# Performance work log

Measured on AMD Instinct MI355X. Metric: run time of the kernel, lower is better.

The kernel has to match this reference:

```python
import jax, jax.numpy as jnp
import numpy as np

N = 100000   # num entities / tail rows
D_IN = 128
D_OUT = 128
R = 8        # num relations
E = 131072   # edges per relation
B = 32768    # head entities per relation


def setup_inputs() -> dict:
    key = jax.random.key(0)
    ks = jax.random.split(key, 8)
    x = jax.random.normal(ks[0], (N, D_IN), dtype=jnp.float32)
    tail_rep = jax.random.normal(ks[1], (N, D_IN), dtype=jnp.float32)
    # Linear(in, out, bias=False) weight: [out, in], xavier-ish scale
    W = jax.random.normal(ks[2], (D_OUT, D_IN), dtype=jnp.float32) * (1.414 / np.sqrt(D_IN))
    # match_matrix embedding -> per-relation [in, out] matrices
    rel_W = jax.random.normal(ks[3], (R, D_IN, D_OUT), dtype=jnp.float32) * (1.0 / np.sqrt(D_IN))
    edge_weights = jax.random.uniform(ks[4], (R, E), dtype=jnp.float32)
    edge_rows = jax.random.randint(ks[5], (R, E), 0, B, dtype=jnp.int32)
    edge_cols = jax.random.randint(ks[6], (R, E), 0, N, dtype=jnp.int32)
    # head_indice: unique global entity ids per relation (torch code assigns by index)
    rng = np.random.default_rng(0)
    head = np.stack([rng.choice(N, size=B, replace=False) for _ in range(R)]).astype(np.int32)
    head_indice = jnp.asarray(head)
    return {"x": x, "tail_rep": tail_rep, "W": W, "rel_W": rel_W,
            "edge_weights": edge_weights, "edge_rows": edge_rows,
            "edge_cols": edge_cols, "head_indice": head_indice}


def reference(x, tail_rep, W, rel_W, edge_weights, edge_rows, edge_cols, head_indice):
    # emb_all = original_map(input)
    emb_all = x @ W.T                                   # [N, D_OUT]
    # per-relation dense transform of all tails: tail_rep @ rel_W[r]
    transformed = jnp.einsum('ni,rio->rno', tail_rep, rel_W)   # [R, N, D_OUT]
    # sparse.mm(sp_edge_e, all_rep_h): gather tail rows per edge, weight, segment-sum by local head row
    gathered = jnp.take_along_axis(transformed, edge_cols[:, :, None], axis=1)  # [R, E, D_OUT]
    contrib = edge_weights[:, :, None] * gathered                                # [R, E, D_OUT]
    seg = lambda c, rows: jax.ops.segment_sum(c, rows, num_segments=B)
    new_rep = jax.vmap(seg)(contrib, edge_rows)                                  # [R, B, D_OUT]
    # emb_all[ent_indice] = rel_update + emb_all[ent_indice]  (per relation, sequentially) == scatter-add
    emb_all = emb_all.at[head_indice.reshape(-1)].add(new_rep.reshape(-1, D_OUT))
    # activate=True
    return jax.nn.relu(emb_all)
```

## Files before the change

kernel.cpp:

```cpp
#include <hip/hip_runtime.h>
#include <hip/hip_bf16.h>

#define D_DIM 128
#define N_ENT 100000
#define R_REL 8
#define E_EDGE 131072
#define B_HEAD 32768
#define NH_PAD 100352
#define MAXE (R_REL * E_EDGE)

typedef __attribute__((ext_vector_type(8))) short short8v;
typedef __attribute__((ext_vector_type(16))) float f32x16;
typedef unsigned int uint;
typedef unsigned short ushort;

union BF8 {
  short8v v;
  __hip_bfloat16 h[8];
};

__device__ inline ushort bfbits(float x) {
  union { __hip_bfloat16 h; ushort u; } c;
  c.h = __float2bfloat16(x);
  return c.u;
}
__device__ inline float bflo(uint p) { return __uint_as_float(p << 16); }
__device__ inline float bfhi(uint p) { return __uint_as_float(p & 0xffff0000u); }

__global__ __launch_bounds__(256) void setup(int* __restrict__ cnt_e,
                                             int* __restrict__ inv,
                                             const float* __restrict__ W,
                                             const float* __restrict__ relW,
                                             short8v* __restrict__ WhS,
                                             const float* __restrict__ tail,
                                             short8v* __restrict__ tailb) {
  int bid = blockIdx.x;
  int tid = threadIdx.x;
  if (bid < 3136) {
    int i = bid * 256 + tid;
    if (i < R_REL * B_HEAD) cnt_e[i] = 0;
    inv[i] = -1;
  } else if (bid < 3208) {
    int b = bid - 3136;
    int mat = b >> 3;
    int idx = (b & 7) * 256 + tid;
    int o = idx & 127, ks = idx >> 7;
    float v[8];
    if (mat == 0) {
      const float* src = W + o * D_DIM + ks * 8;
#pragma unroll
      for (int j = 0; j < 8; ++j) v[j] = src[j];
    } else {
      const float* src =
          relW + (size_t)(mat - 1) * D_DIM * D_DIM + (ks * 8) * D_DIM + o;
#pragma unroll
      for (int j = 0; j < 8; ++j) v[j] = src[j * D_DIM];
    }
    BF8 h;
#pragma unroll
    for (int j = 0; j < 8; ++j) h.h[j] = __float2bfloat16(v[j]);
    WhS[(size_t)mat * 2048 + idx] = h.v;
  } else {
    int i = (bid - 3208) * 256 + tid;
    const float4* s = (const float4*)tail + (size_t)i * 2;
    float4 a = s[0], b = s[1];
    BF8 h;
    h.h[0] = __float2bfloat16(a.x); h.h[1] = __float2bfloat16(a.y);
    h.h[2] = __float2bfloat16(a.z); h.h[3] = __float2bfloat16(a.w);
    h.h[4] = __float2bfloat16(b.x); h.h[5] = __float2bfloat16(b.y);
    h.h[6] = __float2bfloat16(b.z); h.h[7] = __float2bfloat16(b.w);
    tailb[i] = h.v;
  }
}

__global__ __launch_bounds__(256) void hist_inv(const int* __restrict__ erow,
                                                const int* __restrict__ head,
                                                int* __restrict__ cnt,
                                                int* __restrict__ inv) {
  int bid = blockIdx.x;
  if (bid < 4096) {
    int r = bid >> 9;
    int e = (bid & 511) * 256 + threadIdx.x;
    int row = erow[(size_t)r * E_EDGE + e];
    atomicAdd(cnt + r * B_HEAD + row, 1);
  } else {
    int i = (bid - 4096) * 256 + threadIdx.x;
    int r = i >> 15;
    inv[r * NH_PAD + head[i]] = i & (B_HEAD - 1);
  }
}

__global__ __launch_bounds__(256) void scan_blk(const int* __restrict__ cnt,
                                                int* __restrict__ cur,
                                                int* __restrict__ bsum) {
  int b = blockIdx.x, t = threadIdx.x;
  int4 v = ((const int4*)cnt)[b * 256 + t];
  int s = v.x + v.y + v.z + v.w;
  __shared__ int ps[256];
  ps[t] = s;
  __syncthreads();
  for (int off = 1; off < 256; off <<= 1) {
    int u = (t >= off) ? ps[t - off] : 0;
    __syncthreads();
    ps[t] += u;
    __syncthreads();
  }
  int base = ps[t] - s;
  int4 o;
  o.x = base; o.y = base + v.x; o.z = o.y + v.y; o.w = o.z + v.z;
  ((int4*)cur)[b * 256 + t] = o;
  if (t == 255) bsum[b] = ps[255];
}

__global__ __launch_bounds__(256) void scan_bsum(int* __restrict__ bsum) {
  int t = threadIdx.x;
  int s = bsum[t];
  __shared__ int ps[256];
  ps[t] = s;
  __syncthreads();
  for (int off = 1; off < 256; off <<= 1) {
    int u = (t >= off) ? ps[t - off] : 0;
    __syncthreads();
    ps[t] += u;
    __syncthreads();
  }
  bsum[t] = ps[t] - s;
}

__global__ __launch_bounds__(256) void scatter_edges(const int* __restrict__ erow,
                                                     const int* __restrict__ ecol,
                                                     const float* __restrict__ ew,
                                                     int* __restrict__ cur,
                                                     const int* __restrict__ bsum,
                                                     int2* __restrict__ sColW) {
  int r = blockIdx.y;
  int e = blockIdx.x * 256 + threadIdx.x;
  size_t idx = (size_t)r * E_EDGE + e;
  int row = erow[idx];
  int gi = r * B_HEAD + row;
  int pos = atomicAdd(cur + gi, 1) + bsum[gi >> 10];
  sColW[pos] = make_int2(ecol[idx], __float_as_int(ew[idx]));
}

__global__ __launch_bounds__(256) void csr_agg(const uint* __restrict__ tailb,
                                               const int* __restrict__ cur_e,
                                               const int* __restrict__ cnt_e,
                                               const int* __restrict__ bsum,
                                               const int2* __restrict__ sColW,
                                               uint* __restrict__ aggb, int r0) {
  int base = (blockIdx.x << 3) + ((threadIdx.x >> 6) << 1);
  int lane = threadIdx.x & 63;
  int li = lane & 7;
  int f0 = r0 * B_HEAD + base, f1 = f0 + 1;
  int cn0 = cnt_e[f0], cn1 = cnt_e[f1];
  int s0 = cur_e[f0] - cn0 + bsum[f0 >> 10];
  int s1 = cur_e[f1] - cn1 + bsum[f1 >> 10];
  float a0x = 0.f, a0y = 0.f, a1x = 0.f, a1y = 0.f;
  int rounds = ((cn0 > cn1 ? cn0 : cn1) + 7) >> 3;
  for (int rr = 0; rr < rounds; ++rr) {
    int k = rr << 3;
    int i0 = k + li; if (i0 > cn0 - 1) i0 = cn0 > 0 ? cn0 - 1 : 0;
    int i1 = k + li; if (i1 > cn1 - 1) i1 = cn1 > 0 ? cn1 - 1 : 0;
    int g0 = s0 + i0; if (g0 > MAXE - 1) g0 = MAXE - 1;
    int g1 = s1 + i1; if (g1 > MAXE - 1) g1 = MAXE - 1;
    int2 ea = sColW[g0];
    int2 eb = sColW[g1];
#pragma unroll
    for (int j = 0; j < 8; ++j) {
      if (k + j < cn0) {
        int col = __shfl(ea.x, j, 8);
        float w = __int_as_float(__shfl(ea.y, j, 8));
        uint t = tailb[(size_t)col * 64 + lane];
        a0x += w * bflo(t); a0y += w * bfhi(t);
      }
      if (k + j < cn1) {
        int col = __shfl(eb.x, j, 8);
        float w = __int_as_float(__shfl(eb.y, j, 8));
        uint t = tailb[(size_t)col * 64 + lane];
        a1x += w * bflo(t); a1y += w * bfhi(t);
      }
    }
  }
  aggb[(size_t)base * 64 + lane] = (uint)bfbits(a0x) | ((uint)bfbits(a0y) << 16);
  aggb[(size_t)(base + 1) * 64 + lane] = (uint)bfbits(a1x) | ((uint)bfbits(a1y) << 16);
}

__global__ __launch_bounds__(256) void gemm_all(const float* __restrict__ x,
                                                const ushort* __restrict__ aggb,
                                                const short8v* __restrict__ WhS,
                                                float* __restrict__ out,
                                                ushort* __restrict__ updb, int r0,
                                                int nxb) {
  __shared__ short8v wlds[16][128];
  int tid = threadIdx.x;
  int bid = blockIdx.x;
  bool xpart = (bid < nxb);
  int mat, rowbase, relloc = 0;
  if (xpart) {
    mat = 0;
    rowbase = bid * 128;
  } else {
    int b = bid - nxb;
    relloc = b >> 8;
    mat = 1 + r0 + relloc;
    rowbase = (b & 255) * 128;
  }
  const short8v* Bsrc = WhS + (size_t)mat * 2048;
#pragma unroll
  for (int it = 0; it < 8; ++it) {
    int e = it * 256 + tid;
    wlds[e >> 7][e & 127] = Bsrc[e];
  }
  int w = tid >> 6, lane = tid & 63, lrow = lane & 31, lsel = lane >> 5;
  int arow = rowbase + w * 32 + lrow;
  f32x16 acc[4] = {};
  __syncthreads();

  if (xpart) {
    int arowc = (arow < N_ENT) ? arow : (N_ENT - 1);
    const float4* Arow = (const float4*)(x + (size_t)arowc * D_DIM);
#pragma unroll
    for (int kk = 0; kk < 8; ++kk) {
      float4 a0 = Arow[kk * 4 + lsel * 2];
      float4 a1 = Arow[kk * 4 + lsel * 2 + 1];
      BF8 ah;
      ah.h[0] = __float2bfloat16(a0.x); ah.h[1] = __float2bfloat16(a0.y);
      ah.h[2] = __float2bfloat16(a0.z); ah.h[3] = __float2bfloat16(a0.w);
      ah.h[4] = __float2bfloat16(a1.x); ah.h[5] = __float2bfloat16(a1.y);
      ah.h[6] = __float2bfloat16(a1.z); ah.h[7] = __float2bfloat16(a1.w);
      int ks = kk * 2 + lsel;
#pragma unroll
      for (int n = 0; n < 4; ++n)
        acc[n] = __builtin_amdgcn_mfma_f32_32x32x16_bf16(ah.v, wlds[ks][n * 32 + lrow],
                                                         acc[n], 0, 0, 0);
    }
    int wrow0 = rowbase + w * 32;
#pragma unroll
    for (int reg = 0; reg < 16; ++reg) {
      int srow = wrow0 + (reg & 3) + 8 * (reg >> 2) + 4 * lsel;
      if (srow < N_ENT) {
        float* orow = out + (size_t)srow * D_DIM;
#pragma unroll
        for (int n = 0; n < 4; ++n) orow[n * 32 + lrow] = acc[n][reg];
      }
    }
  } else {
    const short8v* Arow =
        (const short8v*)(aggb + ((size_t)relloc * B_HEAD + arow) * D_DIM);
#pragma unroll
    for (int kk = 0; kk < 8; ++kk) {
      short8v a = Arow[kk * 2 + lsel];
      int ks = kk * 2 + lsel;
#pragma unroll
      for (int n = 0; n < 4; ++n)
        acc[n] = __builtin_amdgcn_mfma_f32_32x32x16_bf16(a, wlds[ks][n * 32 + lrow],
                                                         acc[n], 0, 0, 0);
    }
    int wrow0 = rowbase + w * 32;
    ushort* ubase = updb + (size_t)relloc * B_HEAD * D_DIM;
#pragma unroll
    for (int reg = 0; reg < 16; ++reg) {
      int srow = wrow0 + (reg & 3) + 8 * (reg >> 2) + 4 * lsel;
      ushort* urow = ubase + (size_t)srow * D_DIM;
#pragma unroll
      for (int n = 0; n < 4; ++n) urow[n * 32 + lrow] = bfbits(acc[n][reg]);
    }
  }
}

__global__ __launch_bounds__(256) void final_add(const int* __restrict__ inv,
                                                 const ushort* __restrict__ updb,
                                                 float* __restrict__ out, int r0,
                                                 int c, int doRelu) {
  int n = blockIdx.x * 8 + (threadIdx.x >> 5);
  int lane = threadIdx.x & 31;
  if (n >= N_ENT) return;
  float4* o4 = (float4*)out + (size_t)n * 32 + lane;
  float4 v = *o4;
  for (int k = 0; k < c; ++k) {
    int row = inv[(r0 + k) * NH_PAD + n];
    if (row >= 0) {
      uint2 u = ((const uint2*)updb)[((size_t)k * B_HEAD + row) * 32 + lane];
      v.x += bflo(u.x); v.y += bfhi(u.x);
      v.z += bflo(u.y); v.w += bfhi(u.y);
    }
  }
  if (doRelu) {
    v.x = fmaxf(v.x, 0.f); v.y = fmaxf(v.y, 0.f);
    v.z = fmaxf(v.z, 0.f); v.w = fmaxf(v.w, 0.f);
  }
  *o4 = v;
}

extern "C" void kernel_launch(void* const* d_in, const int* in_sizes, int n_in,
                              void* d_out, int out_size, void* d_ws, size_t ws_size,
                              hipStream_t stream) {
  const float* x = (const float*)d_in[0];
  const float* tail = (const float*)d_in[1];
  const float* W = (const float*)d_in[2];
  const float* relW = (const float*)d_in[3];
  const float* ew = (const float*)d_in[4];
  const int* erow = (const int*)d_in[5];
  const int* ecol = (const int*)d_in[6];
  const int* head = (const int*)d_in[7];
  float* out = (float*)d_out;

  char* p = (char*)d_ws;
  short8v* WhS = (short8v*)p;   p += (size_t)(R_REL + 1) * 2048 * 16;
  short8v* tailb = (short8v*)p; p += (size_t)N_ENT * D_DIM * 2;
  int* cnt_e = (int*)p;         p += (size_t)R_REL * B_HEAD * 4;
  int* cur_e = (int*)p;         p += (size_t)R_REL * B_HEAD * 4;
  int* inv = (int*)p;           p += (size_t)R_REL * NH_PAD * 4;
  int* bsum = (int*)p;          p += 256 * 4;
  int2* sColW = (int2*)p;       p += (size_t)R_REL * E_EDGE * 8;
  char* dyn = p;
  size_t fixed = (size_t)(p - (char*)d_ws);
  size_t per_rel = (size_t)B_HEAD * D_DIM * 2 * 2;
  size_t avail = (ws_size > fixed) ? ws_size - fixed : 0;
  int chunk = (int)(avail / per_rel);
  if (chunk > R_REL) chunk = R_REL;
  if (chunk < 1) chunk = 1;
  ushort* aggb = (ushort*)dyn;
  ushort* updb = (ushort*)(dyn + (size_t)chunk * B_HEAD * D_DIM * 2);

  const int NXB = (N_ENT + 127) / 128;

  setup<<<dim3(3136 + 72 + 6250), 256, 0, stream>>>(cnt_e, inv, W, relW, WhS, tail,
                                                    tailb);
  hist_inv<<<dim3(4096 + R_REL * B_HEAD / 256), 256, 0, stream>>>(erow, head, cnt_e,
                                                                  inv);
  scan_blk<<<dim3(256), 256, 0, stream>>>(cnt_e, cur_e, bsum);
  scan_bsum<<<dim3(1), 256, 0, stream>>>(bsum);
  scatter_edges<<<dim3(E_EDGE / 256, R_REL), 256, 0, stream>>>(erow, ecol, ew, cur_e,
                                                               bsum, sColW);

  for (int r0 = 0; r0 < R_REL; r0 += chunk) {
    int c = (R_REL - r0 < chunk) ? (R_REL - r0) : chunk;
    csr_agg<<<dim3(c * B_HEAD / 8), 256, 0, stream>>>(
        (const uint*)tailb, cur_e, cnt_e, bsum, sColW, (uint*)aggb, r0);
    int nxb = (r0 == 0) ? NXB : 0;
    gemm_all<<<dim3(nxb + 256 * c), 256, 0, stream>>>(x, aggb, WhS, out, updb, r0,
                                                      nxb);
    final_add<<<dim3((N_ENT + 7) / 8), 256, 0, stream>>>(inv, updb, out, r0, c,
                                                         (r0 + c == R_REL) ? 1 : 0);
  }
}
```

Measured before the change: 310.8 us.

## Fuse CSR aggregation with per-relation GEMM and merge scan kernels

The sparse aggregation now writes each block's 16 aggregated rows into LDS, and the same block multiplies them by the relation matrix with 16x16x32 MFMA. This removes the global round trip of the bf16 aggregate buffer and the per-chunk loop. The x-projection GEMM becomes its own kernel, and the final add applies all relations and ReLU in one pass. The block-sum scan is folded into scan_blk using a last-block atomic counter, which saves one launch. The trade-offs are small per-block GEMM tiles that reload B from global memory, and the assumption that the workspace can hold updates for all 8 relations at once, since the chunking fallback is gone.

```diff
diff --git a/kernel.cpp b/kernel.cpp
--- a/kernel.cpp
+++ b/kernel.cpp
@@ -8,8 +8,10 @@
 #define B_HEAD 32768
 #define NH_PAD 100352
 #define MAXE (R_REL * E_EDGE)
+#define LDSW 68
 
 typedef __attribute__((ext_vector_type(8))) short short8v;
+typedef __attribute__((ext_vector_type(4))) float f32x4;
 typedef __attribute__((ext_vector_type(16))) float f32x16;
 typedef unsigned int uint;
 typedef unsigned short ushort;
@@ -29,6 +31,7 @@
 
 __global__ __launch_bounds__(256) void setup(int* __restrict__ cnt_e,
                                              int* __restrict__ inv,
+                                             int* __restrict__ done,
                                              const float* __restrict__ W,
                                              const float* __restrict__ relW,
                                              short8v* __restrict__ WhS,
@@ -36,6 +39,7 @@
                                              short8v* __restrict__ tailb) {
   int bid = blockIdx.x;
   int tid = threadIdx.x;
+  if (bid == 0 && tid == 0) *done = 0;
   if (bid < 3136) {
     int i = bid * 256 + tid;
     if (i < R_REL * B_HEAD) cnt_e[i] = 0;
@@ -92,7 +96,8 @@
 
 __global__ __launch_bounds__(256) void scan_blk(const int* __restrict__ cnt,
                                                 int* __restrict__ cur,
-                                                int* __restrict__ bsum) {
+                                                int* __restrict__ bsum,
+                                                int* __restrict__ done) {
   int b = blockIdx.x, t = threadIdx.x;
   int4 v = ((const int4*)cnt)[b * 256 + t];
   int s = v.x + v.y + v.z + v.w;
@@ -110,21 +115,23 @@
   o.x = base; o.y = base + v.x; o.z = o.y + v.y; o.w = o.z + v.z;
   ((int4*)cur)[b * 256 + t] = o;
   if (t == 255) bsum[b] = ps[255];
-}
-
-__global__ __launch_bounds__(256) void scan_bsum(int* __restrict__ bsum) {
-  int t = threadIdx.x;
-  int s = bsum[t];
-  __shared__ int ps[256];
-  ps[t] = s;
+  __threadfence();
+  __shared__ int isLast;
+  if (t == 0) isLast = (atomicAdd(done, 1) == 255);
   __syncthreads();
-  for (int off = 1; off < 256; off <<= 1) {
-    int u = (t >= off) ? ps[t - off] : 0;
+  if (isLast) {
+    __threadfence();
+    int sb = bsum[t];
+    ps[t] = sb;
     __syncthreads();
-    ps[t] += u;
-    __syncthreads();
-  }
-  bsum[t] = ps[t] - s;
+    for (int off = 1; off < 256; off <<= 1) {
+      int u = (t >= off) ? ps[t - off] : 0;
+      __syncthreads();
+      ps[t] += u;
+      __syncthreads();
+    }
+    bsum[t] = ps[t] - sb;
+  }
 }
 
 __global__ __launch_bounds__(256) void scatter_edges(const int* __restrict__ erow,
@@ -142,16 +149,18 @@
   sColW[pos] = make_int2(ecol[idx], __float_as_int(ew[idx]));
 }
 
-__global__ __launch_bounds__(256) void csr_agg(const uint* __restrict__ tailb,
-                                               const int* __restrict__ cur_e,
-                                               const int* __restrict__ cnt_e,
-                                               const int* __restrict__ bsum,
-                                               const int2* __restrict__ sColW,
-                                               uint* __restrict__ aggb, int r0) {
-  int base = (blockIdx.x << 3) + ((threadIdx.x >> 6) << 1);
-  int lane = threadIdx.x & 63;
-  int li = lane & 7;
-  int f0 = r0 * B_HEAD + base, f1 = f0 + 1;
+__global__ __launch_bounds__(512, 8) void fused_agg_gemm(
+    const uint* __restrict__ tailb, const int* __restrict__ cur_e,
+    const int* __restrict__ cnt_e, const int* __restrict__ bsum,
+    const int2* __restrict__ sColW, const short8v* __restrict__ WhS,
+    ushort* __restrict__ updb) {
+  __shared__ uint alds[16 * LDSW];
+  int tid = threadIdx.x;
+  int w = tid >> 6, lane = tid & 63, li = lane & 7;
+  int rel = blockIdx.y;
+  int rowbase = blockIdx.x << 4;
+  int base = rowbase + (w << 1);
+  int f0 = rel * B_HEAD + base, f1 = f0 + 1;
   int cn0 = cnt_e[f0], cn1 = cnt_e[f1];
   int s0 = cur_e[f0] - cn0 + bsum[f0 >> 10];
   int s1 = cur_e[f1] - cn1 + bsum[f1 >> 10];
@@ -169,126 +178,101 @@
     for (int j = 0; j < 8; ++j) {
       if (k + j < cn0) {
         int col = __shfl(ea.x, j, 8);
-        float w = __int_as_float(__shfl(ea.y, j, 8));
+        float wt = __int_as_float(__shfl(ea.y, j, 8));
         uint t = tailb[(size_t)col * 64 + lane];
-        a0x += w * bflo(t); a0y += w * bfhi(t);
+        a0x += wt * bflo(t); a0y += wt * bfhi(t);
       }
       if (k + j < cn1) {
         int col = __shfl(eb.x, j, 8);
-        float w = __int_as_float(__shfl(eb.y, j, 8));
+        float wt = __int_as_float(__shfl(eb.y, j, 8));
         uint t = tailb[(size_t)col * 64 + lane];
-        a1x += w * bflo(t); a1y += w * bfhi(t);
+        a1x += wt * bflo(t); a1y += wt * bfhi(t);
       }
     }
   }
-  aggb[(size_t)base * 64 + lane] = (uint)bfbits(a0x) | ((uint)bfbits(a0y) << 16);
-  aggb[(size_t)(base + 1) * 64 + lane] = (uint)bfbits(a1x) | ((uint)bfbits(a1y) << 16);
-}
-
-__global__ __launch_bounds__(256) void gemm_all(const float* __restrict__ x,
-                                                const ushort* __restrict__ aggb,
-                                                const short8v* __restrict__ WhS,
-                                                float* __restrict__ out,
-                                                ushort* __restrict__ updb, int r0,
-                                                int nxb) {
+  alds[(w * 2 + 0) * LDSW + lane] = (uint)bfbits(a0x) | ((uint)bfbits(a0y) << 16);
+  alds[(w * 2 + 1) * LDSW + lane] = (uint)bfbits(a1x) | ((uint)bfbits(a1y) << 16);
+  __syncthreads();
+
+  int kg = lane >> 4, cl = lane & 15;
+  int ct = w * 16;
+  const short8v* Bm = WhS + (size_t)(1 + rel) * 2048;
+  f32x4 acc = {0.f, 0.f, 0.f, 0.f};
+#pragma unroll
+  for (int kk = 0; kk < 4; ++kk) {
+    short8v a = *(const short8v*)&alds[cl * LDSW + kk * 16 + kg * 4];
+    short8v b = Bm[(kk * 4 + kg) * 128 + ct + cl];
+    acc = __builtin_amdgcn_mfma_f32_16x16x32_bf16(a, b, acc, 0, 0, 0);
+  }
+  ushort* ubase = updb + ((size_t)rel * B_HEAD + rowbase) * D_DIM;
+#pragma unroll
+  for (int reg = 0; reg < 4; ++reg)
+    ubase[(size_t)(kg * 4 + reg) * D_DIM + ct + cl] = bfbits(acc[reg]);
+}
+
+__global__ __launch_bounds__(256) void gemm_x(const float* __restrict__ x,
+                                              const short8v* __restrict__ WhS,
+                                              float* __restrict__ out) {
   __shared__ short8v wlds[16][128];
   int tid = threadIdx.x;
-  int bid = blockIdx.x;
-  bool xpart = (bid < nxb);
-  int mat, rowbase, relloc = 0;
-  if (xpart) {
-    mat = 0;
-    rowbase = bid * 128;
-  } else {
-    int b = bid - nxb;
-    relloc = b >> 8;
-    mat = 1 + r0 + relloc;
-    rowbase = (b & 255) * 128;
-  }
-  const short8v* Bsrc = WhS + (size_t)mat * 2048;
+  int rowbase = blockIdx.x * 128;
 #pragma unroll
   for (int it = 0; it < 8; ++it) {
     int e = it * 256 + tid;
-    wlds[e >> 7][e & 127] = Bsrc[e];
+    wlds[e >> 7][e & 127] = WhS[e];
   }
   int w = tid >> 6, lane = tid & 63, lrow = lane & 31, lsel = lane >> 5;
   int arow = rowbase + w * 32 + lrow;
+  int arowc = (arow < N_ENT) ? arow : (N_ENT - 1);
+  const float4* Arow = (const float4*)(x + (size_t)arowc * D_DIM);
   f32x16 acc[4] = {};
   __syncthreads();
-
-  if (xpart) {
-    int arowc = (arow < N_ENT) ? arow : (N_ENT - 1);
-    const float4* Arow = (const float4*)(x + (size_t)arowc * D_DIM);
-#pragma unroll
-    for (int kk = 0; kk < 8; ++kk) {
-      float4 a0 = Arow[kk * 4 + lsel * 2];
-      float4 a1 = Arow[kk * 4 + lsel * 2 + 1];
-      BF8 ah;
-      ah.h[0] = __float2bfloat16(a0.x); ah.h[1] = __float2bfloat16(a0.y);
-      ah.h[2] = __float2bfloat16(a0.z); ah.h[3] = __float2bfloat16(a0.w);
-      ah.h[4] = __float2bfloat16(a1.x); ah.h[5] = __float2bfloat16(a1.y);
-      ah.h[6] = __float2bfloat16(a1.z); ah.h[7] = __float2bfloat16(a1.w);
-      int ks = kk * 2 + lsel;
-#pragma unroll
-      for (int n = 0; n < 4; ++n)
-        acc[n] = __builtin_amdgcn_mfma_f32_32x32x16_bf16(ah.v, wlds[ks][n * 32 + lrow],
-                                                         acc[n], 0, 0, 0);
-    }
-    int wrow0 = rowbase + w * 32;
-#pragma unroll
-    for (int reg = 0; reg < 16; ++reg) {
-      int srow = wrow0 + (reg & 3) + 8 * (reg >> 2) + 4 * lsel;
-      if (srow < N_ENT) {
-        float* orow = out + (size_t)srow * D_DIM;
-#pragma unroll
-        for (int n = 0; n < 4; ++n) orow[n * 32 + lrow] = acc[n][reg];
-      }
-    }
-  } else {
-    const short8v* Arow =
-        (const short8v*)(aggb + ((size_t)relloc * B_HEAD + arow) * D_DIM);
-#pragma unroll
-    for (int kk = 0; kk < 8; ++kk) {
-      short8v a = Arow[kk * 2 + lsel];
-      int ks = kk * 2 + lsel;
-#pragma unroll
-      for (int n = 0; n < 4; ++n)
-        acc[n] = __builtin_amdgcn_mfma_f32_32x32x16_bf16(a, wlds[ks][n * 32 + lrow],
-                                                         acc[n], 0, 0, 0);
-    }
-    int wrow0 = rowbase + w * 32;
-    ushort* ubase = updb + (size_t)relloc * B_HEAD * D_DIM;
-#pragma unroll
-    for (int reg = 0; reg < 16; ++reg) {
-      int srow = wrow0 + (reg & 3) + 8 * (reg >> 2) + 4 * lsel;
-      ushort* urow = ubase + (size_t)srow * D_DIM;
-#pragma unroll
-      for (int n = 0; n < 4; ++n) urow[n * 32 + lrow] = bfbits(acc[n][reg]);
+#pragma unroll
+  for (int kk = 0; kk < 8; ++kk) {
+    float4 a0 = Arow[kk * 4 + lsel * 2];
+    float4 a1 = Arow[kk * 4 + lsel * 2 + 1];
+    BF8 ah;
+    ah.h[0] = __float2bfloat16(a0.x); ah.h[1] = __float2bfloat16(a0.y);
+    ah.h[2] = __float2bfloat16(a0.z); ah.h[3] = __float2bfloat16(a0.w);
+    ah.h[4] = __float2bfloat16(a1.x); ah.h[5] = __float2bfloat16(a1.y);
+    ah.h[6] = __float2bfloat16(a1.z); ah.h[7] = __float2bfloat16(a1.w);
+    int ks = kk * 2 + lsel;
+#pragma unroll
+    for (int n = 0; n < 4; ++n)
+      acc[n] = __builtin_amdgcn_mfma_f32_32x32x16_bf16(ah.v, wlds[ks][n * 32 + lrow],
+                                                       acc[n], 0, 0, 0);
+  }
+  int wrow0 = rowbase + w * 32;
+#pragma unroll
+  for (int reg = 0; reg < 16; ++reg) {
+    int srow = wrow0 + (reg & 3) + 8 * (reg >> 2) + 4 * lsel;
+    if (srow < N_ENT) {
+      float* orow = out + (size_t)srow * D_DIM;
+#pragma unroll
+      for (int n = 0; n < 4; ++n) orow[n * 32 + lrow] = acc[n][reg];
     }
   }
 }
 
 __global__ __launch_bounds__(256) void final_add(const int* __restrict__ inv,
                                                  const ushort* __restrict__ updb,
-                                                 float* __restrict__ out, int r0,
-                                                 int c, int doRelu) {
+                                                 float* __restrict__ out) {
   int n = blockIdx.x * 8 + (threadIdx.x >> 5);
   int lane = threadIdx.x & 31;
   if (n >= N_ENT) return;
   float4* o4 = (float4*)out + (size_t)n * 32 + lane;
   float4 v = *o4;
-  for (int k = 0; k < c; ++k) {
-    int row = inv[(r0 + k) * NH_PAD + n];
+#pragma unroll
+  for (int k = 0; k < R_REL; ++k) {
+    int row = inv[k * NH_PAD + n];
     if (row >= 0) {
       uint2 u = ((const uint2*)updb)[((size_t)k * B_HEAD + row) * 32 + lane];
       v.x += bflo(u.x); v.y += bfhi(u.x);
       v.z += bflo(u.y); v.w += bfhi(u.y);
     }
   }
-  if (doRelu) {
-    v.x = fmaxf(v.x, 0.f); v.y = fmaxf(v.y, 0.f);
-    v.z = fmaxf(v.z, 0.f); v.w = fmaxf(v.w, 0.f);
-  }
+  v.x = fmaxf(v.x, 0.f); v.y = fmaxf(v.y, 0.f);
+  v.z = fmaxf(v.z, 0.f); v.w = fmaxf(v.w, 0.f);
   *o4 = v;
 }
 
@@ -312,36 +296,19 @@
   int* cur_e = (int*)p;         p += (size_t)R_REL * B_HEAD * 4;
   int* inv = (int*)p;           p += (size_t)R_REL * NH_PAD * 4;
   int* bsum = (int*)p;          p += 256 * 4;
+  int* done = (int*)p;          p += 16;
   int2* sColW = (int2*)p;       p += (size_t)R_REL * E_EDGE * 8;
-  char* dyn = p;
-  size_t fixed = (size_t)(p - (char*)d_ws);
-  size_t per_rel = (size_t)B_HEAD * D_DIM * 2 * 2;
-  size_t avail = (ws_size > fixed) ? ws_size - fixed : 0;
-  int chunk = (int)(avail / per_rel);
-  if (chunk > R_REL) chunk = R_REL;
-  if (chunk < 1) chunk = 1;
-  ushort* aggb = (ushort*)dyn;
-  ushort* updb = (ushort*)(dyn + (size_t)chunk * B_HEAD * D_DIM * 2);
-
-  const int NXB = (N_ENT + 127) / 128;
-
-  setup<<<dim3(3136 + 72 + 6250), 256, 0, stream>>>(cnt_e, inv, W, relW, WhS, tail,
-                                                    tailb);
+  ushort* updb = (ushort*)p;
+
+  setup<<<dim3(3136 + 72 + 6250), 256, 0, stream>>>(cnt_e, inv, done, W, relW, WhS,
+                                                    tail, tailb);
   hist_inv<<<dim3(4096 + R_REL * B_HEAD / 256), 256, 0, stream>>>(erow, head, cnt_e,
                                                                   inv);
-  scan_blk<<<dim3(256), 256, 0, stream>>>(cnt_e, cur_e, bsum);
-  scan_bsum<<<dim3(1), 256, 0, stream>>>(bsum);
+  scan_blk<<<dim3(256), 256, 0, stream>>>(cnt_e, cur_e, bsum, done);
   scatter_edges<<<dim3(E_EDGE / 256, R_REL), 256, 0, stream>>>(erow, ecol, ew, cur_e,
                                                                bsum, sColW);
-
-  for (int r0 = 0; r0 < R_REL; r0 += chunk) {
-    int c = (R_REL - r0 < chunk) ? (R_REL - r0) : chunk;
-    csr_agg<<<dim3(c * B_HEAD / 8), 256, 0, stream>>>(
-        (const uint*)tailb, cur_e, cnt_e, bsum, sColW, (uint*)aggb, r0);
-    int nxb = (r0 == 0) ? NXB : 0;
-    gemm_all<<<dim3(nxb + 256 * c), 256, 0, stream>>>(x, aggb, WhS, out, updb, r0,
-                                                      nxb);
-    final_add<<<dim3((N_ENT + 7) / 8), 256, 0, stream>>>(inv, updb, out, r0, c,
-                                                         (r0 + c == R_REL) ? 1 : 0);
-  }
-}
+  fused_agg_gemm<<<dim3(B_HEAD / 16, R_REL), 512, 0, stream>>>(
+      (const uint*)tailb, cur_e, cnt_e, bsum, sColW, WhS, updb);
+  gemm_x<<<dim3((N_ENT + 127) / 128), 256, 0, stream>>>(x, WhS, out);
+  final_add<<<dim3((N_ENT + 7) / 8), 256, 0, stream>>>(inv, updb, out);
+}
```

Result: slower. 328.8 us (+5.8%).
